# Optimization experiments

Measured on AMD Instinct MI355X. Metric: run time of the kernel, lower is better.

## Reference

```python
import jax, jax.numpy as jnp
import numpy as np

N_HEADS = 16


def setup_inputs() -> dict:
    key = jax.random.key(0)
    k1, k2, k3 = jax.random.split(key, 3)
    S, dim = 4096, 2048
    x = jax.random.normal(k1, (S, dim), dtype=jnp.float32)
    w_qkv = jax.random.normal(k2, (dim, 3 * dim), dtype=jnp.float32) * 0.02
    w_o = jax.random.normal(k3, (dim, dim), dtype=jnp.float32) * 0.02
    return {"x": x, "w_qkv": w_qkv, "w_o": w_o}


def reference(x, w_qkv, w_o):
    S, dim = x.shape
    H = N_HEADS
    D = dim // H
    # fused QKV projection, split into q/k/v each of width dim
    qkv = x @ w_qkv                       # (S, 3*dim)
    q, k, v = jnp.split(qkv, 3, axis=-1)  # each (S, dim)
    q = q.reshape(S, H, D).transpose(1, 0, 2)  # (H, S, D)
    k = k.reshape(S, H, D).transpose(1, 0, 2)
    v = v.reshape(S, H, D).transpose(1, 0, 2)
    scale = 1.0 / np.sqrt(D).astype(np.float32)
    scores = jnp.einsum("hqd,hkd->hqk", q, k) * scale  # (H, S, S)
    # original mask: tril(full(-inf), k=1); positions with mask==0 (j > i+1) are disallowed
    idx = jnp.arange(S)
    allowed = idx[None, :] <= idx[:, None] + 1  # (S, S), j <= i+1
    neg_inf = jnp.asarray(-jnp.inf, dtype=scores.dtype)
    scores = jnp.where(allowed[None, :, :], scores, neg_inf)
    p = jax.nn.softmax(scores, axis=-1)
    o = jnp.einsum("hqk,hkd->hqd", p, v)      # (H, S, D)
    o = o.transpose(1, 0, 2).reshape(S, dim)  # (S, dim)
    return o @ w_o
```

## Files before the change

### kernel.cpp

```cpp
#include <hip/hip_runtime.h>
#include <stdint.h>

#define S_LEN 4096
#define DIM   2048
#define NH    16
#define HD    128
#define N3    6144

typedef unsigned short u16;
typedef __attribute__((ext_vector_type(8))) short bfrag;
typedef __attribute__((ext_vector_type(4))) float ffrag;

__device__ __forceinline__ u16 f2bf(float f) {
  union { float f; unsigned u; } v; v.f = f;
  unsigned r = v.u + 0x7fffu + ((v.u >> 16) & 1u);
  return (u16)(r >> 16);
}

__device__ __forceinline__ void gload16(const void* g, void* l) {
  __builtin_amdgcn_global_load_lds((const __attribute__((address_space(1))) void*)g,
                                   (__attribute__((address_space(3))) void*)l, 16, 0, 0);
}

__global__ void k_cvt(const float* __restrict__ in, u16* __restrict__ out, int n8) {
  int i = blockIdx.x * blockDim.x + threadIdx.x;
  if (i >= n8) return;
  const float4* p = (const float4*)(in + (size_t)i * 8);
  float4 a = p[0], b = p[1];
  bfrag o;
  o[0] = (short)f2bf(a.x); o[1] = (short)f2bf(a.y);
  o[2] = (short)f2bf(a.z); o[3] = (short)f2bf(a.w);
  o[4] = (short)f2bf(b.x); o[5] = (short)f2bf(b.y);
  o[6] = (short)f2bf(b.z); o[7] = (short)f2bf(b.w);
  *(bfrag*)(out + (size_t)i * 8) = o;
}

__global__ void k_trcvt(const float* __restrict__ in, u16* __restrict__ out,
                        int rows, int cols) {
  __shared__ float t[32][33];
  int c0 = blockIdx.x * 32, r0 = blockIdx.y * 32;
  int tx = threadIdx.x, ty = threadIdx.y;
  #pragma unroll
  for (int i = ty; i < 32; i += 8)
    t[i][tx] = in[(size_t)(r0 + i) * cols + c0 + tx];
  __syncthreads();
  #pragma unroll
  for (int i = ty; i < 32; i += 8)
    out[(size_t)(c0 + i) * rows + r0 + tx] = f2bf(t[tx][i]);
}

__global__ void k_trv(const u16* __restrict__ qkv, u16* __restrict__ vt) {
  __shared__ u16 t[32][34];
  int c0 = blockIdx.x * 32, r0 = blockIdx.y * 32;
  int tx = threadIdx.x, ty = threadIdx.y;
  #pragma unroll
  for (int i = ty; i < 32; i += 8)
    t[i][tx] = qkv[(size_t)(r0 + i) * N3 + 2 * DIM + c0 + tx];
  __syncthreads();
  #pragma unroll
  for (int i = ty; i < 32; i += 8)
    vt[(size_t)(c0 + i) * S_LEN + r0 + tx] = t[tx][i];
}

template<int OUT_BF16>
__global__ __launch_bounds__(256) void k_gemm(const u16* __restrict__ A,
                                              const u16* __restrict__ Bt,
                                              void* __restrict__ C,
                                              int M, int N, int K) {
  __shared__ __align__(16) u16 Al[128 * 64];
  __shared__ __align__(16) u16 Bl[128 * 64];
  const int tid = threadIdx.x;
  const int lane = tid & 63;
  const int w = tid >> 6, wr = w >> 1, wc = w & 1;
  const int fr = lane & 15, fq = lane >> 4;

  int nwg = gridDim.x, bid = blockIdx.x;
  int qq = nwg >> 3, r8 = nwg & 7;
  int xcd = bid & 7, ord = bid >> 3;
  int sb = (xcd < r8 ? xcd * (qq + 1) : r8 * (qq + 1) + (xcd - r8) * qq) + ord;
  const int nbx = N >> 7;
  const int bx = sb % nbx, by = sb / nbx;
  const size_t row0 = (size_t)by << 7, col0 = (size_t)bx << 7;

  const int srow = tid >> 3;
  const int scb  = (tid & 7) << 4;

  ffrag acc[4][4] = {};

  for (int k0 = 0; k0 < K; k0 += 64) {
    __syncthreads();
    #pragma unroll
    for (int r = 0; r < 4; ++r) {
      int trow = r * 32 + srow;
      int cb = scb ^ ((trow & 7) << 4);
      gload16(A + (row0 + trow) * K + k0 + (cb >> 1),
              (char*)Al + r * 4096 + w * 1024);
    }
    #pragma unroll
    for (int r = 0; r < 4; ++r) {
      int trow = r * 32 + srow;
      int cb = scb ^ ((trow & 7) << 4);
      gload16(Bt + (col0 + trow) * K + k0 + (cb >> 1),
              (char*)Bl + r * 4096 + w * 1024);
    }
    __syncthreads();
    #pragma unroll
    for (int kk = 0; kk < 2; ++kk) {
      bfrag af[4], bf[4];
      #pragma unroll
      for (int m = 0; m < 4; ++m) {
        int row = wr * 64 + m * 16 + fr;
        af[m] = *(const bfrag*)((const char*)Al + row * 128 +
                                ((kk * 64 + fq * 16) ^ ((row & 7) << 4)));
      }
      #pragma unroll
      for (int n = 0; n < 4; ++n) {
        int row = wc * 64 + n * 16 + fr;
        bf[n] = *(const bfrag*)((const char*)Bl + row * 128 +
                                ((kk * 64 + fq * 16) ^ ((row & 7) << 4)));
      }
      #pragma unroll
      for (int m = 0; m < 4; ++m)
        #pragma unroll
        for (int n = 0; n < 4; ++n)
          acc[m][n] = __builtin_amdgcn_mfma_f32_16x16x32_bf16(af[m], bf[n], acc[m][n], 0, 0, 0);
    }
  }
  #pragma unroll
  for (int m = 0; m < 4; ++m) {
    size_t grow = row0 + wr * 64 + m * 16 + fq * 4;
    #pragma unroll
    for (int n = 0; n < 4; ++n) {
      size_t gcol = col0 + wc * 64 + n * 16 + fr;
      #pragma unroll
      for (int r = 0; r < 4; ++r) {
        if (OUT_BF16) ((u16*)C)[(grow + r) * N + gcol] = f2bf(acc[m][n][r]);
        else          ((float*)C)[(grow + r) * N + gcol] = acc[m][n][r];
      }
    }
  }
}

__global__ __launch_bounds__(512) void k_attn(const u16* __restrict__ qkv,
                                              const u16* __restrict__ vt,
                                              u16* __restrict__ o) {
  __shared__ __align__(16) u16 Kl[64 * 128];
  __shared__ __align__(16) u16 Vl[128 * 64];
  __shared__ __align__(16) u16 Pl[8][16 * 64];
  const int tid = threadIdx.x;
  const int lane = tid & 63;
  const int wq = tid >> 6;
  const int fr = lane & 15, fq = lane >> 4;
  const int qt = blockIdx.x, h = blockIdx.y;
  const int q0 = qt << 7;

  bfrag qf[4];
  {
    const u16* qrow = qkv + (size_t)(q0 + wq * 16 + fr) * N3 + h * HD + fq * 8;
    #pragma unroll
    for (int kk = 0; kk < 4; ++kk)
      qf[kk] = *(const bfrag*)(qrow + kk * 32);
  }
  float mrow[4] = {-1e30f, -1e30f, -1e30f, -1e30f};
  float lrow[4] = {0.f, 0.f, 0.f, 0.f};
  ffrag oacc[8] = {};

  int ntiles = (q0 + 192) >> 6;
  if (ntiles > (S_LEN >> 6)) ntiles = S_LEN >> 6;
  const u16* kbase = qkv + DIM + (size_t)h * HD;
  const u16* vbase = vt + (size_t)h * HD * S_LEN;
  const float scale = 0.088388347648318447f;

  for (int jt = 0; jt < ntiles; ++jt) {
    const int j0 = jt << 6;
    __syncthreads();
    #pragma unroll
    for (int r = 0; r < 2; ++r) {
      int slot = r * 512 + tid;
      int trow = slot >> 4;
      int cb = ((slot & 15) << 4) ^ ((trow & 7) << 4);
      gload16(kbase + (size_t)(j0 + trow) * N3 + (cb >> 1),
              (char*)Kl + r * 8192 + wq * 1024);
    }
    #pragma unroll
    for (int r = 0; r < 2; ++r) {
      int slot = r * 512 + tid;
      int trow = slot >> 3;
      int cb = ((slot & 7) << 4) ^ ((trow & 7) << 4);
      gload16(vbase + (size_t)trow * S_LEN + j0 + (cb >> 1),
              (char*)Vl + r * 8192 + wq * 1024);
    }
    __syncthreads();

    ffrag sacc[4] = {};
    #pragma unroll
    for (int n = 0; n < 4; ++n) {
      int row = n * 16 + fr;
      #pragma unroll
      for (int kk = 0; kk < 4; ++kk) {
        bfrag kf = *(const bfrag*)((const char*)Kl + row * 256 +
                                   ((kk * 64 + fq * 16) ^ ((row & 7) << 4)));
        sacc[n] = __builtin_amdgcn_mfma_f32_16x16x32_bf16(qf[kk], kf, sacc[n], 0, 0, 0);
      }
    }
    float pmax[4] = {-1e30f, -1e30f, -1e30f, -1e30f};
    #pragma unroll
    for (int n = 0; n < 4; ++n) {
      int j = j0 + n * 16 + fr;
      #pragma unroll
      for (int r = 0; r < 4; ++r) {
        int i = q0 + wq * 16 + fq * 4 + r;
        float s = sacc[n][r] * scale;
        if (j > i + 1) s = -1e30f;
        sacc[n][r] = s;
        pmax[r] = fmaxf(pmax[r], s);
      }
    }
    #pragma unroll
    for (int r = 0; r < 4; ++r)
      #pragma unroll
      for (int off = 1; off < 16; off <<= 1)
        pmax[r] = fmaxf(pmax[r], __shfl_xor(pmax[r], off));

    float alpha[4], rsum[4];
    #pragma unroll
    for (int r = 0; r < 4; ++r) {
      float mnew = fmaxf(mrow[r], pmax[r]);
      alpha[r] = __expf(mrow[r] - mnew);
      mrow[r] = mnew;
      rsum[r] = 0.f;
    }
    u16* pl = (u16*)Pl[wq];
    #pragma unroll
    for (int n = 0; n < 4; ++n) {
      #pragma unroll
      for (int r = 0; r < 4; ++r) {
        float p = __expf(sacc[n][r] - mrow[r]);
        rsum[r] += p;
        int prow = fq * 4 + r;
        int pcb = ((n * 16 + fr) << 1) ^ ((prow & 7) << 4);
        *(u16*)((char*)pl + prow * 128 + pcb) = f2bf(p);
      }
    }
    #pragma unroll
    for (int r = 0; r < 4; ++r) {
      #pragma unroll
      for (int off = 1; off < 16; off <<= 1)
        rsum[r] += __shfl_xor(rsum[r], off);
      lrow[r] = lrow[r] * alpha[r] + rsum[r];
    }
    #pragma unroll
    for (int d = 0; d < 8; ++d)
      #pragma unroll
      for (int r = 0; r < 4; ++r)
        oacc[d][r] *= alpha[r];

    asm volatile("s_waitcnt lgkmcnt(0)" ::: "memory");

    #pragma unroll
    for (int kf = 0; kf < 2; ++kf) {
      bfrag pf = *(const bfrag*)((const char*)pl + fr * 128 +
                                 ((kf * 64 + fq * 16) ^ ((fr & 7) << 4)));
      #pragma unroll
      for (int d = 0; d < 8; ++d) {
        int row = d * 16 + fr;
        bfrag vf = *(const bfrag*)((const char*)Vl + row * 128 +
                                   ((kf * 64 + fq * 16) ^ ((row & 7) << 4)));
        oacc[d] = __builtin_amdgcn_mfma_f32_16x16x32_bf16(pf, vf, oacc[d], 0, 0, 0);
      }
    }
  }
  float linv[4];
  #pragma unroll
  for (int r = 0; r < 4; ++r) linv[r] = 1.f / lrow[r];
  #pragma unroll
  for (int d = 0; d < 8; ++d) {
    #pragma unroll
    for (int r = 0; r < 4; ++r) {
      size_t row = q0 + wq * 16 + fq * 4 + r;
      size_t col = (size_t)h * HD + d * 16 + fr;
      o[row * DIM + col] = f2bf(oacc[d][r] * linv[r]);
    }
  }
}

extern "C" void kernel_launch(void* const* d_in, const int* in_sizes, int n_in,
                              void* d_out, int out_size, void* d_ws, size_t ws_size,
                              hipStream_t stream) {
  const float* x     = (const float*)d_in[0];
  const float* w_qkv = (const float*)d_in[1];
  const float* w_o   = (const float*)d_in[2];
  float* out = (float*)d_out;

  u16* xb    = (u16*)d_ws;
  u16* wqkvT = xb    + (size_t)S_LEN * DIM;
  u16* woT   = wqkvT + (size_t)DIM * N3;
  u16* qkvb  = woT   + (size_t)DIM * DIM;
  u16* vtb   = qkvb  + (size_t)S_LEN * N3;
  u16* ob    = vtb   + (size_t)DIM * S_LEN;

  k_cvt<<<(S_LEN * DIM / 8 + 255) / 256, 256, 0, stream>>>(x, xb, S_LEN * DIM / 8);
  k_trcvt<<<dim3(N3 / 32, DIM / 32), dim3(32, 8), 0, stream>>>(w_qkv, wqkvT, DIM, N3);
  k_trcvt<<<dim3(DIM / 32, DIM / 32), dim3(32, 8), 0, stream>>>(w_o, woT, DIM, DIM);

  k_gemm<1><<<(S_LEN / 128) * (N3 / 128), 256, 0, stream>>>(xb, wqkvT, qkvb, S_LEN, N3, DIM);
  k_trv<<<dim3(DIM / 32, S_LEN / 32), dim3(32, 8), 0, stream>>>(qkvb, vtb);
  k_attn<<<dim3(S_LEN / 128, NH), 512, 0, stream>>>(qkvb, vtb, ob);
  k_gemm<0><<<(S_LEN / 128) * (DIM / 128), 256, 0, stream>>>(ob, woT, out, S_LEN, DIM, DIM);
}
```

Baseline: 636.0 us.

## Double-buffer K/V tiles, skip masked warp tiles, lazy rescale, remap attention blocks

The attention kernel now double-buffers K/V tiles in shared memory so the next tile's global-to-LDS loads overlap compute, with one barrier per iteration. Warps whose rows lie entirely before a tile skip its compute, and masking runs only on diagonal tiles. Softmax uses hardware exp2 with a folded scale, and rescaling of the running max is skipped unless the max grows past a threshold. Blocks are remapped so long and short causal rows interleave across heads for load balance. The cost is doubled LDS use, which may reduce occupancy.

```diff
diff --git a/kernel.cpp b/kernel.cpp
--- a/kernel.cpp
+++ b/kernel.cpp
@@ -15,6 +15,12 @@
   union { float f; unsigned u; } v; v.f = f;
   unsigned r = v.u + 0x7fffu + ((v.u >> 16) & 1u);
   return (u16)(r >> 16);
+}
+
+__device__ __forceinline__ float exp2_hw(float x) {
+  float r;
+  asm("v_exp_f32 %0, %1" : "=v"(r) : "v"(x));
+  return r;
 }
 
 __device__ __forceinline__ void gload16(const void* g, void* l) {
@@ -144,24 +150,30 @@
 __global__ __launch_bounds__(512) void k_attn(const u16* __restrict__ qkv,
                                               const u16* __restrict__ vt,
                                               u16* __restrict__ o) {
-  __shared__ __align__(16) u16 Kl[64 * 128];
-  __shared__ __align__(16) u16 Vl[128 * 64];
+  __shared__ __align__(16) u16 Kl[2][64 * 128];
+  __shared__ __align__(16) u16 Vl[2][128 * 64];
   __shared__ __align__(16) u16 Pl[8][16 * 64];
   const int tid = threadIdx.x;
   const int lane = tid & 63;
   const int wq = tid >> 6;
   const int fr = lane & 15, fq = lane >> 4;
-  const int qt = blockIdx.x, h = blockIdx.y;
+
+  const int bid = blockIdx.x;
+  const int sb = (bid & 7) * 64 + (bid >> 3);
+  const int h = sb >> 5;
+  const int tt = sb & 31;
+  const int qt = (h & 1) ? tt : (31 - tt);
   const int q0 = qt << 7;
+  const int iw0 = q0 + wq * 16;
 
   bfrag qf[4];
   {
-    const u16* qrow = qkv + (size_t)(q0 + wq * 16 + fr) * N3 + h * HD + fq * 8;
+    const u16* qrow = qkv + (size_t)(iw0 + fr) * N3 + h * HD + fq * 8;
     #pragma unroll
     for (int kk = 0; kk < 4; ++kk)
       qf[kk] = *(const bfrag*)(qrow + kk * 32);
   }
-  float mrow[4] = {-1e30f, -1e30f, -1e30f, -1e30f};
+  float mrow[4] = {-3e38f, -3e38f, -3e38f, -3e38f};
   float lrow[4] = {0.f, 0.f, 0.f, 0.f};
   ffrag oacc[8] = {};
 
@@ -169,115 +181,137 @@
   if (ntiles > (S_LEN >> 6)) ntiles = S_LEN >> 6;
   const u16* kbase = qkv + DIM + (size_t)h * HD;
   const u16* vbase = vt + (size_t)h * HD * S_LEN;
-  const float scale = 0.088388347648318447f;
+  const float sc2 = 0.088388347648318447f * 1.4426950408889634f;
+
+#define STAGE_KV(J0, KD, VD)                                               \
+  do {                                                                     \
+    _Pragma("unroll")                                                      \
+    for (int r = 0; r < 2; ++r) {                                          \
+      int slot = r * 512 + tid;                                            \
+      int trow = slot >> 4;                                                \
+      int cb = ((slot & 15) << 4) ^ ((trow & 7) << 4);                     \
+      gload16(kbase + (size_t)((J0) + trow) * N3 + (cb >> 1),              \
+              (char*)(KD) + r * 8192 + wq * 1024);                         \
+    }                                                                      \
+    _Pragma("unroll")                                                      \
+    for (int r = 0; r < 2; ++r) {                                          \
+      int slot = r * 512 + tid;                                            \
+      int trow = slot >> 3;                                                \
+      int cb = ((slot & 7) << 4) ^ ((trow & 7) << 4);                      \
+      gload16(vbase + (size_t)trow * S_LEN + (J0) + (cb >> 1),             \
+              (char*)(VD) + r * 8192 + wq * 1024);                         \
+    }                                                                      \
+  } while (0)
+
+  STAGE_KV(0, Kl[0], Vl[0]);
+  __syncthreads();
+  int cur = 0;
 
   for (int jt = 0; jt < ntiles; ++jt) {
     const int j0 = jt << 6;
+    if (jt + 1 < ntiles)
+      STAGE_KV((jt + 1) << 6, Kl[cur ^ 1], Vl[cur ^ 1]);
+
+    const bool active = (j0 <= iw0 + 16);
+    if (active) {
+      const char* Kc = (const char*)Kl[cur];
+      const char* Vc = (const char*)Vl[cur];
+      ffrag sacc[4] = {};
+      #pragma unroll
+      for (int n = 0; n < 4; ++n) {
+        int row = n * 16 + fr;
+        #pragma unroll
+        for (int kk = 0; kk < 4; ++kk) {
+          bfrag kf = *(const bfrag*)(Kc + row * 256 +
+                                     ((kk * 64 + fq * 16) ^ ((row & 7) << 4)));
+          sacc[n] = __builtin_amdgcn_mfma_f32_16x16x32_bf16(qf[kk], kf, sacc[n], 0, 0, 0);
+        }
+      }
+      const bool needmask = (j0 + 63) > (iw0 + 1);
+      float pmax[4] = {-3e38f, -3e38f, -3e38f, -3e38f};
+      #pragma unroll
+      for (int n = 0; n < 4; ++n) {
+        int j = j0 + n * 16 + fr;
+        #pragma unroll
+        for (int r = 0; r < 4; ++r) {
+          float s = sacc[n][r];
+          if (needmask) {
+            int i = iw0 + fq * 4 + r;
+            if (j > i + 1) s = -3e38f;
+            sacc[n][r] = s;
+          }
+          pmax[r] = fmaxf(pmax[r], s);
+        }
+      }
+      #pragma unroll
+      for (int r = 0; r < 4; ++r)
+        #pragma unroll
+        for (int off = 1; off < 16; off <<= 1)
+          pmax[r] = fmaxf(pmax[r], __shfl_xor(pmax[r], off));
+
+      float needv = fmaxf(fmaxf(pmax[0] - mrow[0], pmax[1] - mrow[1]),
+                          fmaxf(pmax[2] - mrow[2], pmax[3] - mrow[3]));
+      if (!__all(needv * sc2 <= 8.0f)) {
+        #pragma unroll
+        for (int r = 0; r < 4; ++r) {
+          float mnew = fmaxf(mrow[r], pmax[r]);
+          float alpha = exp2_hw((mrow[r] - mnew) * sc2);
+          mrow[r] = mnew;
+          lrow[r] *= alpha;
+          #pragma unroll
+          for (int d = 0; d < 8; ++d) oacc[d][r] *= alpha;
+        }
+      }
+
+      u16* pl = (u16*)Pl[wq];
+      float rsum[4] = {0.f, 0.f, 0.f, 0.f};
+      #pragma unroll
+      for (int n = 0; n < 4; ++n) {
+        #pragma unroll
+        for (int r = 0; r < 4; ++r) {
+          float p = exp2_hw((sacc[n][r] - mrow[r]) * sc2);
+          rsum[r] += p;
+          int prow = fq * 4 + r;
+          int pcb = ((n * 16 + fr) << 1) ^ ((prow & 7) << 4);
+          *(u16*)((char*)pl + prow * 128 + pcb) = f2bf(p);
+        }
+      }
+      #pragma unroll
+      for (int r = 0; r < 4; ++r) {
+        #pragma unroll
+        for (int off = 1; off < 16; off <<= 1)
+          rsum[r] += __shfl_xor(rsum[r], off);
+        lrow[r] += rsum[r];
+      }
+
+      asm volatile("s_waitcnt lgkmcnt(0)" ::: "memory");
+
+      #pragma unroll
+      for (int kf2 = 0; kf2 < 2; ++kf2) {
+        bfrag pf = *(const bfrag*)((const char*)pl + fr * 128 +
+                                   ((kf2 * 64 + fq * 16) ^ ((fr & 7) << 4)));
+        #pragma unroll
+        for (int d = 0; d < 8; ++d) {
+          int row = d * 16 + fr;
+          bfrag vf = *(const bfrag*)(Vc + row * 128 +
+                                     ((kf2 * 64 + fq * 16) ^ ((row & 7) << 4)));
+          oacc[d] = __builtin_amdgcn_mfma_f32_16x16x32_bf16(pf, vf, oacc[d], 0, 0, 0);
+        }
+      }
+    }
     __syncthreads();
-    #pragma unroll
-    for (int r = 0; r < 2; ++r) {
-      int slot = r * 512 + tid;
-      int trow = slot >> 4;
-      int cb = ((slot & 15) << 4) ^ ((trow & 7) << 4);
-      gload16(kbase + (size_t)(j0 + trow) * N3 + (cb >> 1),
-              (char*)Kl + r * 8192 + wq * 1024);
-    }
-    #pragma unroll
-    for (int r = 0; r < 2; ++r) {
-      int slot = r * 512 + tid;
-      int trow = slot >> 3;
-      int cb = ((slot & 7) << 4) ^ ((trow & 7) << 4);
-      gload16(vbase + (size_t)trow * S_LEN + j0 + (cb >> 1),
-              (char*)Vl + r * 8192 + wq * 1024);
-    }
-    __syncthreads();
-
-    ffrag sacc[4] = {};
-    #pragma unroll
-    for (int n = 0; n < 4; ++n) {
-      int row = n * 16 + fr;
-      #pragma unroll
-      for (int kk = 0; kk < 4; ++kk) {
-        bfrag kf = *(const bfrag*)((const char*)Kl + row * 256 +
-                                   ((kk * 64 + fq * 16) ^ ((row & 7) << 4)));
-        sacc[n] = __builtin_amdgcn_mfma_f32_16x16x32_bf16(qf[kk], kf, sacc[n], 0, 0, 0);
-      }
-    }
-    float pmax[4] = {-1e30f, -1e30f, -1e30f, -1e30f};
-    #pragma unroll
-    for (int n = 0; n < 4; ++n) {
-      int j = j0 + n * 16 + fr;
-      #pragma unroll
-      for (int r = 0; r < 4; ++r) {
-        int i = q0 + wq * 16 + fq * 4 + r;
-        float s = sacc[n][r] * scale;
-        if (j > i + 1) s = -1e30f;
-        sacc[n][r] = s;
-        pmax[r] = fmaxf(pmax[r], s);
-      }
-    }
-    #pragma unroll
-    for (int r = 0; r < 4; ++r)
-      #pragma unroll
-      for (int off = 1; off < 16; off <<= 1)
-        pmax[r] = fmaxf(pmax[r], __shfl_xor(pmax[r], off));
-
-    float alpha[4], rsum[4];
+    cur ^= 1;
+  }
+#undef STAGE_KV
+
+  float linv[4];
+  #pragma unroll
+  for (int r = 0; r < 4; ++r) linv[r] = 1.f / lrow[r];
+  #pragma unroll
+  for (int d = 0; d < 8; ++d) {
     #pragma unroll
     for (int r = 0; r < 4; ++r) {
-      float mnew = fmaxf(mrow[r], pmax[r]);
-      alpha[r] = __expf(mrow[r] - mnew);
-      mrow[r] = mnew;
-      rsum[r] = 0.f;
-    }
-    u16* pl = (u16*)Pl[wq];
-    #pragma unroll
-    for (int n = 0; n < 4; ++n) {
-      #pragma unroll
-      for (int r = 0; r < 4; ++r) {
-        float p = __expf(sacc[n][r] - mrow[r]);
-        rsum[r] += p;
-        int prow = fq * 4 + r;
-        int pcb = ((n * 16 + fr) << 1) ^ ((prow & 7) << 4);
-        *(u16*)((char*)pl + prow * 128 + pcb) = f2bf(p);
-      }
-    }
-    #pragma unroll
-    for (int r = 0; r < 4; ++r) {
-      #pragma unroll
-      for (int off = 1; off < 16; off <<= 1)
-        rsum[r] += __shfl_xor(rsum[r], off);
-      lrow[r] = lrow[r] * alpha[r] + rsum[r];
-    }
-    #pragma unroll
-    for (int d = 0; d < 8; ++d)
-      #pragma unroll
-      for (int r = 0; r < 4; ++r)
-        oacc[d][r] *= alpha[r];
-
-    asm volatile("s_waitcnt lgkmcnt(0)" ::: "memory");
-
-    #pragma unroll
-    for (int kf = 0; kf < 2; ++kf) {
-      bfrag pf = *(const bfrag*)((const char*)pl + fr * 128 +
-                                 ((kf * 64 + fq * 16) ^ ((fr & 7) << 4)));
-      #pragma unroll
-      for (int d = 0; d < 8; ++d) {
-        int row = d * 16 + fr;
-        bfrag vf = *(const bfrag*)((const char*)Vl + row * 128 +
-                                   ((kf * 64 + fq * 16) ^ ((row & 7) << 4)));
-        oacc[d] = __builtin_amdgcn_mfma_f32_16x16x32_bf16(pf, vf, oacc[d], 0, 0, 0);
-      }
-    }
-  }
-  float linv[4];
-  #pragma unroll
-  for (int r = 0; r < 4; ++r) linv[r] = 1.f / lrow[r];
-  #pragma unroll
-  for (int d = 0; d < 8; ++d) {
-    #pragma unroll
-    for (int r = 0; r < 4; ++r) {
-      size_t row = q0 + wq * 16 + fq * 4 + r;
+      size_t row = iw0 + fq * 4 + r;
       size_t col = (size_t)h * HD + d * 16 + fr;
       o[row * DIM + col] = f2bf(oacc[d][r] * linv[r]);
     }
@@ -305,6 +339,6 @@
 
   k_gemm<1><<<(S_LEN / 128) * (N3 / 128), 256, 0, stream>>>(xb, wqkvT, qkvb, S_LEN, N3, DIM);
   k_trv<<<dim3(DIM / 32, S_LEN / 32), dim3(32, 8), 0, stream>>>(qkvb, vtb);
-  k_attn<<<dim3(S_LEN / 128, NH), 512, 0, stream>>>(qkvb, vtb, ob);
+  k_attn<<<512, 512, 0, stream>>>(qkvb, vtb, ob);
   k_gemm<0><<<(S_LEN / 128) * (DIM / 128), 256, 0, stream>>>(ob, woT, out, S_LEN, DIM, DIM);
 }
```

Measured after the change: 585.2 us. 8.0% less time.
